# Performance work log

Measured on AMD Instinct MI355X. Metric: run time of the kernel, lower is better.

Reference implementation:

```python
import jax, jax.numpy as jnp
import numpy as np

B, L, V, E, H = 128, 512, 256, 64, 256


def setup_inputs() -> dict:
    key = jax.random.key(0)
    ks = jax.random.split(key, 8)
    x = jax.random.randint(ks[0], (B, L), 0, V, dtype=jnp.int64)
    hidden = jnp.zeros((B, H), dtype=jnp.float32)  # init_hidden path
    emb = jax.random.normal(ks[1], (V, E), dtype=jnp.float32)  # nn.Embedding table
    W_xh = jax.random.normal(ks[2], (E, H), dtype=jnp.float32) * 0.01
    W_hh = jax.random.normal(ks[3], (H, H), dtype=jnp.float32) * 0.01
    b_h = jnp.zeros((H,), dtype=jnp.float32)
    W_hy_w = jax.random.normal(ks[4], (V, H), dtype=jnp.float32) * (1.0 / np.sqrt(H))  # nn.Linear weight
    W_hy_b = jnp.zeros((V,), dtype=jnp.float32)  # nn.Linear bias
    b_y = jnp.zeros((V,), dtype=jnp.float32)     # extra bias added in forward
    return {"x": x, "hidden": hidden, "emb": emb, "W_xh": W_xh, "W_hh": W_hh,
            "b_h": b_h, "W_hy_w": W_hy_w, "W_hy_b": W_hy_b, "b_y": b_y}


def reference(x, hidden, emb, W_xh, W_hh, b_h, W_hy_w, W_hy_b, b_y):
    # x: [B, L] int -> embed: [B, L, E]
    x_embed = emb[x]
    # time-major for the recurrence: [L, B, E]
    x_tm = jnp.transpose(x_embed, (1, 0, 2))

    def step(h_prev, x_t):
        h_t = jnp.tanh(x_t @ W_xh + h_prev @ W_hh + b_h)
        return h_t, h_t

    final_hidden, hs = jax.lax.scan(step, hidden, x_tm)  # hs: [L, B, H]
    output = jnp.transpose(hs, (1, 0, 2))                # [B, L, H]
    # nn.Linear (weight [V,H] + bias) plus extra b_y
    logits = jnp.einsum('blh,vh->blv', output, W_hy_w) + W_hy_b + b_y
    return logits, final_hidden
```

## Files before the change

kernel.cpp:

```cpp
#include <hip/hip_runtime.h>
#include <hip/hip_bf16.h>
#include <stdint.h>

#define B_ 128
#define L_ 512
#define V_ 256
#define E_ 64
#define H_ 256
#define SC 2.885390081777927f

typedef __attribute__((ext_vector_type(8))) __bf16 bf16x8;
typedef __attribute__((ext_vector_type(4))) float f32x4;
typedef __attribute__((ext_vector_type(8))) unsigned short ushort8;

__device__ __forceinline__ unsigned short f2bf(float f) {
    unsigned int u = __builtin_bit_cast(unsigned int, f);
    u += 0x7fffu + ((u >> 16) & 1u);
    return (unsigned short)(u >> 16);
}

__global__ void prologue_kernel(const float* __restrict__ emb,
                                const float* __restrict__ Wxh,
                                const float* __restrict__ bh,
                                const float* __restrict__ Why,
                                const float* __restrict__ Whyb,
                                const float* __restrict__ by,
                                const float* __restrict__ Whh,
                                float* __restrict__ embW2,
                                unsigned short* __restrict__ whyb16,
                                float* __restrict__ bias,
                                unsigned short* __restrict__ whhT16)
{
    int blk = blockIdx.x, tid = threadIdx.x;
    if (blk < V_) {
        float s = bh[tid];
        #pragma unroll 8
        for (int e = 0; e < E_; ++e)
            s = fmaf(emb[blk * E_ + e], Wxh[e * H_ + tid], s);
        embW2[blk * H_ + tid] = s * SC;
    } else if (blk < 2 * V_) {
        int i = (blk - V_) * 256 + tid;
        whyb16[i] = f2bf(Why[i]);
    } else if (blk == 2 * V_) {
        bias[tid] = Whyb[tid] + by[tid];
    } else {
        int c = blk - (2 * V_ + 1);
        whhT16[c * H_ + tid] = f2bf(Whh[tid * H_ + c] * SC);
    }
}

__global__ __launch_bounds__(256, 1) void rnn_rec_kernel(
    const int* __restrict__ x, const float* __restrict__ hidden,
    const float* __restrict__ embW2, const unsigned short* __restrict__ whhT16,
    unsigned short* __restrict__ hs, float* __restrict__ hfin)
{
    __shared__ unsigned short h_lds[2][16 * 256];

    const int tid  = threadIdx.x;
    const int w    = tid >> 6, lane = tid & 63;
    const int l15  = lane & 15, lhi = lane >> 4;
    const int lhi4 = lhi * 4;
    const int b0   = blockIdx.x * 16;
    char* ldsbase  = (char*)&h_lds[0][0];

    const unsigned swzm = (unsigned)((l15 & 7) << 4);
    const unsigned rb2 = (unsigned)(l15 * 512)
                       + ((unsigned)(lhi * 16) ^ (swzm & 0x30u))
                       + (swzm & 0x40u);
    const unsigned wab0 = (unsigned)(l15 * 512)
                        + (unsigned)(w * 128)
                        + (((unsigned)(lhi * 8)) ^ (swzm & 0x10u))
                        + (swzm & 0x60u);

    bf16x8 afrag[4][8];
    #pragma unroll
    for (int f = 0; f < 4; ++f)
        #pragma unroll
        for (int kt = 0; kt < 8; ++kt)
            afrag[f][kt] = *(const bf16x8*)(whhT16 +
                (w * 64 + f * 16 + l15) * H_ + kt * 32 + lhi * 8);

    for (int i = tid; i < 16 * 256; i += 256) {
        int row = i >> 8, c = i & 255;
        *(unsigned short*)(ldsbase + (row * 512 + ((c * 2) ^ ((row & 7) << 4)))) =
            f2bf(hidden[(b0 + row) * H_ + c]);
    }

    const char* e8 = (const char*)embW2;
    const unsigned go = (unsigned)((w * 64 + lhi4) * 4);
    const int* xp = x + (b0 + l15) * L_ + 2;
    char* hsp = (char*)hs + (size_t)(b0 + l15) * L_ * (H_ * 2) + (w * 64 + lhi4) * 2;

    int xvA = x[(b0 + l15) * L_ + 0];
    f32x4 eA[4], eB[4];
    {
        unsigned v0 = ((unsigned)xvA << 10) + go;
        #pragma unroll
        for (int f = 0; f < 4; ++f)
            eA[f] = *(const f32x4*)(e8 + v0 + f * 64);
    }
    int xvB = x[(b0 + l15) * L_ + 1];

    __syncthreads();

    auto phase = [&](f32x4 (&ec)[4], f32x4 (&en)[4],
                     int xg, int& xf, int CB, bool PG, bool PX, bool FIN)
                     __attribute__((always_inline)) {
        if (PG) {
            unsigned vo = ((unsigned)xg << 10) + go;
            #pragma unroll
            for (int f = 0; f < 4; ++f)
                en[f] = *(const f32x4*)(e8 + vo + f * 64);
        }
        if (PX) { xf = *xp; ++xp; }

        bf16x8 hv[8];
        #pragma unroll
        for (int kt = 0; kt < 8; ++kt)
            hv[kt] = *(const bf16x8*)(ldsbase +
                       (rb2 ^ (unsigned)((kt << 6) | (CB << 13))));

        f32x4 acc[4];
        #pragma unroll
        for (int f = 0; f < 4; ++f) acc[f] = ec[f];

        f32x4 th[4];
        uint2 p[4];

        #pragma unroll
        for (int kt = 0; kt < 8; ++kt)
            acc[0] = __builtin_amdgcn_mfma_f32_16x16x32_bf16(afrag[0][kt], hv[kt], acc[0], 0, 0, 0);

        #pragma unroll
        for (int f = 0; f < 4; ++f) {
            if (f < 3) {
                #pragma unroll
                for (int kt = 0; kt < 8; ++kt)
                    acc[f + 1] = __builtin_amdgcn_mfma_f32_16x16x32_bf16(
                                     afrag[f + 1][kt], hv[kt], acc[f + 1], 0, 0, 0);
            }
            #pragma unroll
            for (int r = 0; r < 4; ++r) {
                float e = __builtin_exp2f(acc[f][r]);
                th[f][r] = 1.0f - 2.0f * __builtin_amdgcn_rcpf(e + 1.0f);
            }
            asm("v_cvt_pk_bf16_f32 %0, %1, %2" : "=v"(p[f].x) : "v"(th[f][0]), "v"(th[f][1]));
            asm("v_cvt_pk_bf16_f32 %0, %1, %2" : "=v"(p[f].y) : "v"(th[f][2]), "v"(th[f][3]));
            *(uint2*)(ldsbase + ((wab0 ^ (unsigned)(f << 5)) + ((CB ^ 1) << 13))) = p[f];
            *(uint2*)(hsp + f * 32) = p[f];
        }
        hsp += 512;

        if (FIN) {
            #pragma unroll
            for (int f = 0; f < 4; ++f)
                *(f32x4*)(hfin + (b0 + l15) * H_ + w * 64 + f * 16 + lhi4) = th[f];
        }

        __builtin_amdgcn_sched_barrier(0);
        asm volatile("s_waitcnt lgkmcnt(0)" ::: "memory");
        __builtin_amdgcn_s_barrier();
        __builtin_amdgcn_sched_barrier(0);
    };

    for (int i = 0; i < 255; ++i) {
        phase(eA, eB, xvB, xvA, 0, true, true, false);
        phase(eB, eA, xvA, xvB, 1, true, true, false);
    }
    phase(eA, eB, xvB, xvA, 0, true, false, false);
    phase(eB, eA, 0, xvB, 1, false, false, true);
}

__global__ __launch_bounds__(256, 1) void logits_kernel(
    const unsigned short* __restrict__ hs,
    const unsigned short* __restrict__ whyb16,
    const float* __restrict__ bias,
    float* __restrict__ logits)
{
    __shared__ unsigned short a_lds[2][32 * 256];

    const int tid = threadIdx.x;
    const int w = tid >> 6, lane = tid & 63;
    const int l15 = lane & 15, lhi = lane >> 4;
    const size_t rowblk = (size_t)blockIdx.x * 256;

    int col[4];
    #pragma unroll
    for (int n = 0; n < 4; ++n) col[n] = w * 64 + n * 16 + l15;

    bf16x8 bfrag[4][8];
    #pragma unroll
    for (int n = 0; n < 4; ++n)
        #pragma unroll
        for (int kt = 0; kt < 8; ++kt)
            bfrag[n][kt] = *(const bf16x8*)(whyb16 + col[n] * H_ + kt * 32 + lhi * 8);

    float bv[4];
    #pragma unroll
    for (int n = 0; n < 4; ++n) bv[n] = bias[col[n]];

    auto swz = [](unsigned row, unsigned inrow) -> unsigned {
        return row * 512u + (inrow ^ ((row & 7u) << 4));
    };

    #pragma unroll
    for (int ii = 0; ii < 4; ++ii) {
        unsigned Lg = (unsigned)(ii * 256 + tid) * 16u;
        unsigned row = Lg >> 9, inrow = Lg & 511u;
        ushort8 v = *(const ushort8*)((const char*)hs +
                     ((rowblk + row) * 512u + inrow));
        *(ushort8*)((char*)a_lds[0] + swz(row, inrow)) = v;
    }
    __syncthreads();

    for (int c = 0; c < 8; ++c) {
        const int cb = c & 1;
        ushort8 vs[4];
        unsigned srow[4], sinrow[4];
        if (c < 7) {
            #pragma unroll
            for (int ii = 0; ii < 4; ++ii) {
                unsigned Lg = (unsigned)(ii * 256 + tid) * 16u;
                srow[ii] = Lg >> 9; sinrow[ii] = Lg & 511u;
                vs[ii] = *(const ushort8*)((const char*)hs +
                          ((rowblk + (size_t)(c + 1) * 32 + srow[ii]) * 512u + sinrow[ii]));
            }
        }

        #pragma unroll
        for (int m = 0; m < 2; ++m) {
            f32x4 acc[4];
            #pragma unroll
            for (int n = 0; n < 4; ++n) acc[n] = f32x4{0.f, 0.f, 0.f, 0.f};
            #pragma unroll
            for (int kt = 0; kt < 8; ++kt) {
                unsigned rl = (unsigned)(m * 16 + l15);
                bf16x8 a = *(const bf16x8*)((const char*)a_lds[cb] +
                            swz(rl, (unsigned)(kt * 64 + lhi * 16)));
                #pragma unroll
                for (int n = 0; n < 4; ++n)
                    acc[n] = __builtin_amdgcn_mfma_f32_16x16x32_bf16(
                                 a, bfrag[n][kt], acc[n], 0, 0, 0);
            }
            size_t grow = rowblk + (size_t)c * 32 + m * 16 + lhi * 4;
            #pragma unroll
            for (int n = 0; n < 4; ++n)
                #pragma unroll
                for (int r = 0; r < 4; ++r)
                    logits[(grow + r) * V_ + col[n]] = acc[n][r] + bv[n];
        }
        if (c < 7) {
            #pragma unroll
            for (int ii = 0; ii < 4; ++ii)
                *(ushort8*)((char*)a_lds[cb ^ 1] + swz(srow[ii], sinrow[ii])) = vs[ii];
        }
        __syncthreads();
    }
}

extern "C" void kernel_launch(void* const* d_in, const int* in_sizes, int n_in,
                              void* d_out, int out_size, void* d_ws, size_t ws_size,
                              hipStream_t stream) {
    const int*   x      = (const int*)d_in[0];
    const float* hidden = (const float*)d_in[1];
    const float* emb    = (const float*)d_in[2];
    const float* Wxh    = (const float*)d_in[3];
    const float* Whh    = (const float*)d_in[4];
    const float* bh     = (const float*)d_in[5];
    const float* Why    = (const float*)d_in[6];
    const float* Whyb   = (const float*)d_in[7];
    const float* by     = (const float*)d_in[8];

    float* out = (float*)d_out;
    char*  ws  = (char*)d_ws;

    unsigned short* hs     = (unsigned short*)ws;
    float*          embW2  = (float*)(ws + 33554432);
    unsigned short* whyb16 = (unsigned short*)(ws + 33816576);
    float*          bias   = (float*)(ws + 33947648);
    unsigned short* whhT16 = (unsigned short*)(ws + 33948672);

    prologue_kernel<<<2 * V_ + 1 + V_, 256, 0, stream>>>(emb, Wxh, bh, Why, Whyb, by, Whh,
                                                         embW2, whyb16, bias, whhT16);
    rnn_rec_kernel<<<B_ / 16, 256, 0, stream>>>(x, hidden, embW2, whhT16,
                                                hs, out + (size_t)B_ * L_ * V_);
    logits_kernel<<<(B_ * L_) / 256, 256, 0, stream>>>(hs, whyb16, bias, out);
}
```

Baseline: 454.2 us.

## Split MFMA accumulation chains and interleave tanh with matrix ops in recurrence step

Each output fragment's 8-deep dependent MFMA chain is split into two independent 4-deep chains (za, zb) that are summed before tanh. This shortens the serial dependency latency on the critical path of the recurrence. The fragments are issued in interleaved pairs, with sched_group_barrier hints that overlap the tanh/VALU work of fragments 0-1 with the MFMAs of fragments 2-3, and the embedding/x prefetch moves after the LDS reads. The cost is extra accumulator registers and one extra add per element.

```diff
diff --git a/kernel.cpp b/kernel.cpp
--- a/kernel.cpp
+++ b/kernel.cpp
@@ -106,13 +106,7 @@
     auto phase = [&](f32x4 (&ec)[4], f32x4 (&en)[4],
                      int xg, int& xf, int CB, bool PG, bool PX, bool FIN)
                      __attribute__((always_inline)) {
-        if (PG) {
-            unsigned vo = ((unsigned)xg << 10) + go;
-            #pragma unroll
-            for (int f = 0; f < 4; ++f)
-                en[f] = *(const f32x4*)(e8 + vo + f * 64);
-        }
-        if (PX) { xf = *xp; ++xp; }
+        const f32x4 zro = {0.f, 0.f, 0.f, 0.f};
 
         bf16x8 hv[8];
         #pragma unroll
@@ -120,35 +114,57 @@
             hv[kt] = *(const bf16x8*)(ldsbase +
                        (rb2 ^ (unsigned)((kt << 6) | (CB << 13))));
 
-        f32x4 acc[4];
-        #pragma unroll
-        for (int f = 0; f < 4; ++f) acc[f] = ec[f];
-
+        if (PG) {
+            unsigned vo = ((unsigned)xg << 10) + go;
+            #pragma unroll
+            for (int f = 0; f < 4; ++f)
+                en[f] = *(const f32x4*)(e8 + vo + f * 64);
+        }
+        if (PX) { xf = *xp; ++xp; }
+
+        f32x4 za[4], zb[4];
         f32x4 th[4];
         uint2 p[4];
 
-        #pragma unroll
-        for (int kt = 0; kt < 8; ++kt)
-            acc[0] = __builtin_amdgcn_mfma_f32_16x16x32_bf16(afrag[0][kt], hv[kt], acc[0], 0, 0, 0);
-
-        #pragma unroll
-        for (int f = 0; f < 4; ++f) {
-            if (f < 3) {
-                #pragma unroll
-                for (int kt = 0; kt < 8; ++kt)
-                    acc[f + 1] = __builtin_amdgcn_mfma_f32_16x16x32_bf16(
-                                     afrag[f + 1][kt], hv[kt], acc[f + 1], 0, 0, 0);
-            }
+        auto tanhw = [&](int f) __attribute__((always_inline)) {
+            f32x4 z;
+            #pragma unroll
+            for (int r = 0; r < 4; ++r) z[r] = za[f][r] + zb[f][r];
             #pragma unroll
             for (int r = 0; r < 4; ++r) {
-                float e = __builtin_exp2f(acc[f][r]);
-                th[f][r] = 1.0f - 2.0f * __builtin_amdgcn_rcpf(e + 1.0f);
+                float e = __builtin_exp2f(z[r]);
+                th[f][r] = fmaf(-2.0f, __builtin_amdgcn_rcpf(e + 1.0f), 1.0f);
             }
             asm("v_cvt_pk_bf16_f32 %0, %1, %2" : "=v"(p[f].x) : "v"(th[f][0]), "v"(th[f][1]));
             asm("v_cvt_pk_bf16_f32 %0, %1, %2" : "=v"(p[f].y) : "v"(th[f][2]), "v"(th[f][3]));
             *(uint2*)(ldsbase + ((wab0 ^ (unsigned)(f << 5)) + ((CB ^ 1) << 13))) = p[f];
             *(uint2*)(hsp + f * 32) = p[f];
-        }
+        };
+
+        #pragma unroll
+        for (int r = 0; r < 4; ++r) {
+            za[0] = __builtin_amdgcn_mfma_f32_16x16x32_bf16(afrag[0][r],     hv[r],     r ? za[0] : ec[0], 0, 0, 0);
+            zb[0] = __builtin_amdgcn_mfma_f32_16x16x32_bf16(afrag[0][r + 4], hv[r + 4], r ? zb[0] : zro,   0, 0, 0);
+            za[1] = __builtin_amdgcn_mfma_f32_16x16x32_bf16(afrag[1][r],     hv[r],     r ? za[1] : ec[1], 0, 0, 0);
+            zb[1] = __builtin_amdgcn_mfma_f32_16x16x32_bf16(afrag[1][r + 4], hv[r + 4], r ? zb[1] : zro,   0, 0, 0);
+        }
+        __builtin_amdgcn_sched_barrier(0);
+
+        #pragma unroll
+        for (int r = 0; r < 4; ++r) {
+            za[2] = __builtin_amdgcn_mfma_f32_16x16x32_bf16(afrag[2][r],     hv[r],     r ? za[2] : ec[2], 0, 0, 0);
+            zb[2] = __builtin_amdgcn_mfma_f32_16x16x32_bf16(afrag[2][r + 4], hv[r + 4], r ? zb[2] : zro,   0, 0, 0);
+            za[3] = __builtin_amdgcn_mfma_f32_16x16x32_bf16(afrag[3][r],     hv[r],     r ? za[3] : ec[3], 0, 0, 0);
+            zb[3] = __builtin_amdgcn_mfma_f32_16x16x32_bf16(afrag[3][r + 4], hv[r + 4], r ? zb[3] : zro,   0, 0, 0);
+            __builtin_amdgcn_sched_group_barrier(0x8, 4, 0);
+            __builtin_amdgcn_sched_group_barrier(0x2, 9, 0);
+        }
+        tanhw(0);
+        tanhw(1);
+        __builtin_amdgcn_sched_barrier(0);
+
+        tanhw(2);
+        tanhw(3);
         hsp += 512;
 
         if (FIN) {
```

Result: no change. 460.2 us (+1.3%).

## Pack two batch tiles per RNN block and interleave MFMA accumulator chains

Applied to the files above, without the earlier changes.

The recurrence kernel now runs 512 threads per block covering 32 batch rows as two 16-row tiles, each with its own double-buffered LDS hidden state. This gives two waves per SIMD so the latency of one tile's serial step chain can be hidden behind the other. The per-step matmul now issues the four independent accumulator chains interleaved instead of one chain at a time, and the embedding and token prefetch loads are issued after the LDS reads. The trade-off is half as many workgroups and CUs in use, a wider block barrier each step, and the two waves sharing one SIMD's MFMA pipe.

```diff
diff --git a/kernel.cpp b/kernel.cpp
--- a/kernel.cpp
+++ b/kernel.cpp
@@ -49,28 +49,32 @@
     }
 }
 
-__global__ __launch_bounds__(256, 1) void rnn_rec_kernel(
+__global__ __launch_bounds__(512)
+__attribute__((amdgpu_waves_per_eu(2, 2)))
+void rnn_rec_kernel(
     const int* __restrict__ x, const float* __restrict__ hidden,
     const float* __restrict__ embW2, const unsigned short* __restrict__ whhT16,
     unsigned short* __restrict__ hs, float* __restrict__ hfin)
 {
-    __shared__ unsigned short h_lds[2][16 * 256];
+    __shared__ unsigned short h_lds[2][2][16 * 256];
 
     const int tid  = threadIdx.x;
     const int w    = tid >> 6, lane = tid & 63;
     const int l15  = lane & 15, lhi = lane >> 4;
     const int lhi4 = lhi * 4;
-    const int b0   = blockIdx.x * 16;
-    char* ldsbase  = (char*)&h_lds[0][0];
+    const int tile = w >> 2, wt = w & 3;
+    const int b0   = blockIdx.x * 32;
+    const int brow = b0 + tile * 16 + l15;
+    const int hb   = wt * 64;
+    char* ldsbase  = (char*)&h_lds[0][0][0];
+    const unsigned tbase = (unsigned)(tile << 14);
 
     const unsigned swzm = (unsigned)((l15 & 7) << 4);
     const unsigned rb2 = (unsigned)(l15 * 512)
                        + ((unsigned)(lhi * 16) ^ (swzm & 0x30u))
-                       + (swzm & 0x40u);
-    const unsigned wab0 = (unsigned)(l15 * 512)
-                        + (unsigned)(w * 128)
-                        + (((unsigned)(lhi * 8)) ^ (swzm & 0x10u))
-                        + (swzm & 0x60u);
+                       + (swzm & 0x40u) + tbase;
+    const unsigned wab0 = (unsigned)(l15 * 512) + tbase
+                        + (((unsigned)(wt * 128 + lhi * 8)) ^ swzm);
 
     bf16x8 afrag[4][8];
     #pragma unroll
@@ -78,20 +82,22 @@
         #pragma unroll
         for (int kt = 0; kt < 8; ++kt)
             afrag[f][kt] = *(const bf16x8*)(whhT16 +
-                (w * 64 + f * 16 + l15) * H_ + kt * 32 + lhi * 8);
-
-    for (int i = tid; i < 16 * 256; i += 256) {
-        int row = i >> 8, c = i & 255;
-        *(unsigned short*)(ldsbase + (row * 512 + ((c * 2) ^ ((row & 7) << 4)))) =
-            f2bf(hidden[(b0 + row) * H_ + c]);
+                (hb + f * 16 + l15) * H_ + kt * 32 + lhi * 8);
+
+    for (int i = tid; i < 32 * 256; i += 512) {
+        int row32 = i >> 8, c = i & 255;
+        int trow = row32 & 15;
+        *(unsigned short*)(ldsbase + ((row32 >> 4) * 16384 + trow * 512 +
+            ((c * 2) ^ ((trow & 7) << 4)))) =
+            f2bf(hidden[(b0 + row32) * H_ + c]);
     }
 
     const char* e8 = (const char*)embW2;
-    const unsigned go = (unsigned)((w * 64 + lhi4) * 4);
-    const int* xp = x + (b0 + l15) * L_ + 2;
-    char* hsp = (char*)hs + (size_t)(b0 + l15) * L_ * (H_ * 2) + (w * 64 + lhi4) * 2;
-
-    int xvA = x[(b0 + l15) * L_ + 0];
+    const unsigned go = (unsigned)((hb + lhi4) * 4);
+    const int* xp = x + brow * L_ + 2;
+    char* hsp = (char*)hs + (size_t)brow * L_ * (H_ * 2) + (hb + lhi4) * 2;
+
+    int xvA = x[brow * L_ + 0];
     f32x4 eA[4], eB[4];
     {
         unsigned v0 = ((unsigned)xvA << 10) + go;
@@ -99,50 +105,45 @@
         for (int f = 0; f < 4; ++f)
             eA[f] = *(const f32x4*)(e8 + v0 + f * 64);
     }
-    int xvB = x[(b0 + l15) * L_ + 1];
+    int xvB = x[brow * L_ + 1];
 
     __syncthreads();
 
     auto phase = [&](f32x4 (&ec)[4], f32x4 (&en)[4],
                      int xg, int& xf, int CB, bool PG, bool PX, bool FIN)
                      __attribute__((always_inline)) {
-        if (PG) {
-            unsigned vo = ((unsigned)xg << 10) + go;
-            #pragma unroll
-            for (int f = 0; f < 4; ++f)
-                en[f] = *(const f32x4*)(e8 + vo + f * 64);
-        }
-        if (PX) { xf = *xp; ++xp; }
-
         bf16x8 hv[8];
         #pragma unroll
         for (int kt = 0; kt < 8; ++kt)
             hv[kt] = *(const bf16x8*)(ldsbase +
                        (rb2 ^ (unsigned)((kt << 6) | (CB << 13))));
 
-        f32x4 acc[4];
-        #pragma unroll
-        for (int f = 0; f < 4; ++f) acc[f] = ec[f];
-
+        if (PG) {
+            unsigned vo = ((unsigned)xg << 10) + go;
+            #pragma unroll
+            for (int f = 0; f < 4; ++f)
+                en[f] = *(const f32x4*)(e8 + vo + f * 64);
+        }
+        if (PX) { xf = *xp; ++xp; }
+
+        f32x4 z0 = ec[0], z1 = ec[1], z2 = ec[2], z3 = ec[3];
+        #pragma unroll
+        for (int kt = 0; kt < 8; ++kt) {
+            z0 = __builtin_amdgcn_mfma_f32_16x16x32_bf16(afrag[0][kt], hv[kt], z0, 0, 0, 0);
+            z1 = __builtin_amdgcn_mfma_f32_16x16x32_bf16(afrag[1][kt], hv[kt], z1, 0, 0, 0);
+            z2 = __builtin_amdgcn_mfma_f32_16x16x32_bf16(afrag[2][kt], hv[kt], z2, 0, 0, 0);
+            z3 = __builtin_amdgcn_mfma_f32_16x16x32_bf16(afrag[3][kt], hv[kt], z3, 0, 0, 0);
+        }
+
+        f32x4 zz[4] = {z0, z1, z2, z3};
         f32x4 th[4];
         uint2 p[4];
-
-        #pragma unroll
-        for (int kt = 0; kt < 8; ++kt)
-            acc[0] = __builtin_amdgcn_mfma_f32_16x16x32_bf16(afrag[0][kt], hv[kt], acc[0], 0, 0, 0);
-
         #pragma unroll
         for (int f = 0; f < 4; ++f) {
-            if (f < 3) {
-                #pragma unroll
-                for (int kt = 0; kt < 8; ++kt)
-                    acc[f + 1] = __builtin_amdgcn_mfma_f32_16x16x32_bf16(
-                                     afrag[f + 1][kt], hv[kt], acc[f + 1], 0, 0, 0);
-            }
             #pragma unroll
             for (int r = 0; r < 4; ++r) {
-                float e = __builtin_exp2f(acc[f][r]);
-                th[f][r] = 1.0f - 2.0f * __builtin_amdgcn_rcpf(e + 1.0f);
+                float e = __builtin_exp2f(zz[f][r]);
+                th[f][r] = fmaf(-2.0f, __builtin_amdgcn_rcpf(e + 1.0f), 1.0f);
             }
             asm("v_cvt_pk_bf16_f32 %0, %1, %2" : "=v"(p[f].x) : "v"(th[f][0]), "v"(th[f][1]));
             asm("v_cvt_pk_bf16_f32 %0, %1, %2" : "=v"(p[f].y) : "v"(th[f][2]), "v"(th[f][3]));
@@ -154,7 +155,7 @@
         if (FIN) {
             #pragma unroll
             for (int f = 0; f < 4; ++f)
-                *(f32x4*)(hfin + (b0 + l15) * H_ + w * 64 + f * 16 + lhi4) = th[f];
+                *(f32x4*)(hfin + brow * H_ + hb + f * 16 + lhi4) = th[f];
         }
 
         __builtin_amdgcn_sched_barrier(0);
@@ -282,7 +283,7 @@
 
     prologue_kernel<<<2 * V_ + 1 + V_, 256, 0, stream>>>(emb, Wxh, bh, Why, Whyb, by, Whh,
                                                          embW2, whyb16, bias, whhT16);
-    rnn_rec_kernel<<<B_ / 16, 256, 0, stream>>>(x, hidden, embW2, whhT16,
+    rnn_rec_kernel<<<B_ / 32, 512, 0, stream>>>(x, hidden, embW2, whhT16,
                                                 hs, out + (size_t)B_ * L_ * V_);
     logits_kernel<<<(B_ * L_) / 256, 256, 0, stream>>>(hs, whyb16, bias, out);
 }
```

After: 925.5 us. 104% more time.
